# Kernel tuning notes

Hardware: AMD Instinct MI355X
Metric: run time of the kernel (lower is better)

The kernel has to match this reference:

```python
import jax, jax.numpy as jnp
import numpy as np

N, E, D, K, B = 50000, 600000, 128, 8, 64
E_DIM = 16  # edge_attr feature dim (hard-coded nn.Linear(16, in_dim))


def setup_inputs() -> dict:
    key = jax.random.key(0)
    ks = jax.random.split(key, 10)
    x = jax.random.normal(ks[0], (N, D), dtype=jnp.float32)
    edge_index = jax.random.randint(ks[1], (2, E), 0, N)
    edge_attr = jax.random.normal(ks[2], (E, E_DIM), dtype=jnp.float32)
    # binary pocket membership mask [N, K]
    pkt_mask = (jax.random.uniform(ks[3], (N, K)) < 0.3).astype(jnp.float32)
    batch = jnp.sort(jax.random.randint(ks[4], (N,), 0, B))
    s = 1.0 / np.sqrt(D)
    We = jax.random.normal(ks[5], (E_DIM, D), dtype=jnp.float32) * (1.0 / np.sqrt(E_DIM))
    be = jnp.zeros((D,), jnp.float32)
    W1 = jax.random.normal(ks[6], (D, D), dtype=jnp.float32) * s
    b1 = jnp.zeros((D,), jnp.float32)
    W2 = jax.random.normal(ks[7], (D, D), dtype=jnp.float32) * s
    b2 = jnp.zeros((D,), jnp.float32)
    eps = jnp.zeros((), jnp.float32)  # GINEConv train_eps init 0
    gamma = jnp.ones((D,), jnp.float32)
    beta = jnp.zeros((D,), jnp.float32)
    Wv = jax.random.normal(ks[8], (D, D), dtype=jnp.float32) * s
    bv = jnp.zeros((D,), jnp.float32)
    return {"x": x, "edge_index": edge_index, "edge_attr": edge_attr,
            "pkt_mask": pkt_mask, "batch": batch,
            "We": We, "be": be, "W1": W1, "b1": b1, "W2": W2, "b2": b2,
            "eps": eps, "gamma": gamma, "beta": beta, "Wv": Wv, "bv": bv}


def reference(x, edge_index, edge_attr, pkt_mask, batch,
              We, be, W1, b1, W2, b2, eps, gamma, beta, Wv, bv):
    src, dst = edge_index[0], edge_index[1]
    # edge_lin: [E,16] -> [E,D]
    edge_emb = edge_attr @ We + be
    # GINEConv: message = relu(x_src + edge_emb), scatter-add at dst
    msg = jax.nn.relu(x[src] + edge_emb)
    agg = jax.ops.segment_sum(msg, dst, num_segments=N)
    h = (1.0 + eps) * x + agg
    x_res = jax.nn.relu(h @ W1 + b1) @ W2 + b2  # nn MLP
    # virtual feedback: pocket-wise masked mean pooling per graph
    xw = x_res[:, None, :] * pkt_mask[:, :, None]          # [N,K,D]
    pocket_sum = jax.ops.segment_sum(xw.reshape(N, K * D), batch,
                                     num_segments=B).reshape(B, K, D)
    pocket_count = jax.ops.segment_sum(pkt_mask, batch, num_segments=B)  # [B,K]
    pocket_mean = pocket_sum / (pocket_count[:, :, None] + 1e-9)
    pocket_emb = pocket_mean @ Wv + bv                      # [B,K,D]
    node_pe = pocket_emb[batch]                             # gather -> [N,K,D]
    x_res = x_res + (node_pe * pkt_mask[:, :, None]).sum(axis=1)
    # LayerNorm (eps=1e-5, population variance as in torch)
    mu = x_res.mean(axis=-1, keepdims=True)
    var = ((x_res - mu) ** 2).mean(axis=-1, keepdims=True)
    y = (x_res - mu) / jnp.sqrt(var + 1e-5) * gamma + beta
    # ReLU activation; dropout is identity in eval mode
    return jax.nn.relu(y)
```

## Files before the change

kernel.cpp:

```cpp
#include <hip/hip_runtime.h>
#include <hip/hip_bf16.h>
#include <stdint.h>

#define D 128
#define K 8
#define BGRAPH 64
#define CH 64
#define GRP 4

__global__ __launch_bounds__(256) void cast_x_kernel(
    const float* __restrict__ x, __hip_bfloat16* __restrict__ xb, int n)
{
    const int i = (blockIdx.x * 256 + threadIdx.x) * 8;
    if (i + 8 > n) return;
    const float4 a = *(const float4*)(x + i);
    const float4 b = *(const float4*)(x + i + 4);
    __hip_bfloat16 v[8];
    v[0] = __float2bfloat16(a.x); v[1] = __float2bfloat16(a.y);
    v[2] = __float2bfloat16(a.z); v[3] = __float2bfloat16(a.w);
    v[4] = __float2bfloat16(b.x); v[5] = __float2bfloat16(b.y);
    v[6] = __float2bfloat16(b.z); v[7] = __float2bfloat16(b.w);
    *(uint4*)(xb + i) = *(const uint4*)v;
}

__global__ __launch_bounds__(256) void hist_kernel(
    const int* __restrict__ dst, int* __restrict__ deg, int E)
{
    const int i = (blockIdx.x * 256 + threadIdx.x) * 4;
    if (i + 4 <= E) {
        const int4 v = *(const int4*)(dst + i);
        atomicAdd(&deg[v.x], 1);
        atomicAdd(&deg[v.y], 1);
        atomicAdd(&deg[v.z], 1);
        atomicAdd(&deg[v.w], 1);
    } else {
        for (int j = i; j < E; ++j) atomicAdd(&deg[dst[j]], 1);
    }
}

__global__ __launch_bounds__(256) void scan_partial_kernel(
    const int* __restrict__ deg, int* __restrict__ bsum, int N)
{
    const int t = threadIdx.x;
    const int base = (blockIdx.x * 256 + t) * 4;
    int s = 0;
    if (base + 4 <= N) {
        const int4 v = *(const int4*)(deg + base);
        s = v.x + v.y + v.z + v.w;
    } else {
        for (int j = base; j < N; ++j) s += deg[j];
    }
    __shared__ int red[256];
    red[t] = s;
    __syncthreads();
    for (int off = 128; off; off >>= 1) {
        if (t < off) red[t] += red[t + off];
        __syncthreads();
    }
    if (t == 0) bsum[blockIdx.x] = red[0];
}

__global__ __launch_bounds__(64) void scan_top_kernel(
    const int* __restrict__ bsum, int* __restrict__ boffs, int nb)
{
    __shared__ int sh[64];
    const int t = threadIdx.x;
    const int v = (t < nb) ? bsum[t] : 0;
    sh[t] = v;
    __syncthreads();
    for (int off = 1; off < 64; off <<= 1) {
        const int u = (t >= off) ? sh[t - off] : 0;
        __syncthreads();
        sh[t] += u;
        __syncthreads();
    }
    if (t < nb) boffs[t] = sh[t] - v;
}

__global__ __launch_bounds__(256) void scan_final_kernel(
    const int* __restrict__ deg, const int* __restrict__ boffs,
    int* __restrict__ cursor, int N)
{
    const int t = threadIdx.x;
    const int base = (blockIdx.x * 256 + t) * 4;
    int v0 = 0, v1 = 0, v2 = 0, v3 = 0;
    if (base + 4 <= N) {
        const int4 v = *(const int4*)(deg + base);
        v0 = v.x; v1 = v.y; v2 = v.z; v3 = v.w;
    } else {
        if (base     < N) v0 = deg[base];
        if (base + 1 < N) v1 = deg[base + 1];
        if (base + 2 < N) v2 = deg[base + 2];
        if (base + 3 < N) v3 = deg[base + 3];
    }
    const int s = v0 + v1 + v2 + v3;
    __shared__ int sh[256];
    sh[t] = s;
    __syncthreads();
    for (int off = 1; off < 256; off <<= 1) {
        const int u = (t >= off) ? sh[t - off] : 0;
        __syncthreads();
        sh[t] += u;
        __syncthreads();
    }
    int ex = boffs[blockIdx.x] + sh[t] - s;
    if (base < N)     { cursor[base]     = ex; } ex += v0;
    if (base + 1 < N) { cursor[base + 1] = ex; } ex += v1;
    if (base + 2 < N) { cursor[base + 2] = ex; } ex += v2;
    if (base + 3 < N) { cursor[base + 3] = ex; }
}

__global__ __launch_bounds__(256) void scatter_kernel(
    const int* __restrict__ src, const int* __restrict__ dst,
    int* __restrict__ cursor, int4* __restrict__ sde, int E)
{
    const int i = blockIdx.x * 256 + threadIdx.x;
    if (i < E) {
        const int sv = src[i];
        const int dv = dst[i];
        const int p = atomicAdd(&cursor[dv], 1);
        sde[p] = make_int4(sv, dv, i, 0);
    }
}

__device__ __forceinline__ void flush_row(
    float* __restrict__ agg, int node, int d, float2 acc, int first, int last)
{
    float* p = agg + (size_t)node * D + d;
    if (node == first || node == last) {
        if (acc.x != 0.f) atomicAdd(p,     acc.x);
        if (acc.y != 0.f) atomicAdd(p + 1, acc.y);
    } else {
        *(float2*)p = acc;
    }
}

__global__ __launch_bounds__(256) void gine_reduce_kernel(
    const __hip_bfloat16* __restrict__ xb, const int4* __restrict__ sde,
    const float* __restrict__ ea, const float* __restrict__ We,
    const float* __restrict__ be, float* __restrict__ agg, int E)
{
    const int wave = threadIdx.x >> 6;
    const int lane = threadIdx.x & 63;
    const int chunk = __builtin_amdgcn_readfirstlane(blockIdx.x * 4 + wave);
    const int e0 = chunk * CH;
    if (e0 >= E) return;
    const int d = lane * 2;
    const int NG = CH / GRP;

    float2 w[16];
    #pragma unroll
    for (int j = 0; j < 16; ++j) w[j] = *(const float2*)(We + j * D + d);
    const float2 bb = *(const float2*)(be + d);

    int4 mcur[GRP], mnext[GRP];
    #pragma unroll
    for (int j = 0; j < GRP; ++j) mcur[j] = sde[e0 + j];
    #pragma unroll
    for (int j = 0; j < GRP; ++j) mnext[j] = sde[e0 + GRP + j];
    __hip_bfloat162 xcur[GRP];
    #pragma unroll
    for (int j = 0; j < GRP; ++j)
        xcur[j] = *(const __hip_bfloat162*)(xb + (size_t)mcur[j].x * D + d);

    const int first = mcur[0].y;
    const int last  = sde[e0 + CH - 1].y;

    float2 acc = make_float2(0.f, 0.f);
    int cur = first;

    for (int g = 0; g < NG; ++g) {
        int4 mnn[GRP] = {};
        __hip_bfloat162 xn[GRP] = {};
        if (g + 2 < NG) {
            #pragma unroll
            for (int j = 0; j < GRP; ++j) mnn[j] = sde[e0 + (g + 2) * GRP + j];
        }
        if (g + 1 < NG) {
            #pragma unroll
            for (int j = 0; j < GRP; ++j)
                xn[j] = *(const __hip_bfloat162*)(xb + (size_t)mnext[j].x * D + d);
        }

        float4 A[GRP][4];
        #pragma unroll
        for (int j = 0; j < GRP; ++j) {
            const float4* p = (const float4*)(ea + (size_t)mcur[j].z * 16);
            A[j][0] = p[0]; A[j][1] = p[1]; A[j][2] = p[2]; A[j][3] = p[3];
        }

        #pragma unroll
        for (int j = 0; j < GRP; ++j) {
            const int dk = mcur[j].y;
            if (dk != cur) {
                flush_row(agg, cur, d, acc, first, last);
                acc = make_float2(0.f, 0.f);
                cur = dk;
            }
            float m0 = bb.x + __bfloat162float(xcur[j].x);
            float m1 = bb.y + __bfloat162float(xcur[j].y);
            const float av[16] = {
                A[j][0].x, A[j][0].y, A[j][0].z, A[j][0].w,
                A[j][1].x, A[j][1].y, A[j][1].z, A[j][1].w,
                A[j][2].x, A[j][2].y, A[j][2].z, A[j][2].w,
                A[j][3].x, A[j][3].y, A[j][3].z, A[j][3].w};
            #pragma unroll
            for (int jj = 0; jj < 16; ++jj) {
                m0 += av[jj] * w[jj].x;
                m1 += av[jj] * w[jj].y;
            }
            acc.x += m0 > 0.f ? m0 : 0.f;
            acc.y += m1 > 0.f ? m1 : 0.f;
        }

        #pragma unroll
        for (int j = 0; j < GRP; ++j) {
            mcur[j] = mnext[j]; mnext[j] = mnn[j]; xcur[j] = xn[j];
        }
    }
    flush_row(agg, cur, d, acc, first, last);
}

#define MT_ROWS 64
#define SH_STR  132
__global__ __launch_bounds__(256) void mlp_kernel(
    const float* __restrict__ x, const float* __restrict__ agg,
    const float* __restrict__ epsp,
    const float* __restrict__ W1, const float* __restrict__ b1,
    const float* __restrict__ W2, const float* __restrict__ b2,
    float* __restrict__ xres, int N)
{
    __shared__ float sh[MT_ROWS * SH_STR];
    const int row0 = blockIdx.x * MT_ROWS;
    const float ep = 1.0f + epsp[0];

    for (int i = threadIdx.x; i < MT_ROWS * D / 4; i += 256) {
        const int flat = i * 4;
        const int r = flat >> 7;
        const int c = flat & (D - 1);
        const int row = row0 + r;
        float4 hv;
        if (row < N) {
            const float4 xv = *(const float4*)(x   + (size_t)row * D + c);
            const float4 av = *(const float4*)(agg + (size_t)row * D + c);
            hv = make_float4(ep * xv.x + av.x, ep * xv.y + av.y,
                             ep * xv.z + av.z, ep * xv.w + av.w);
        } else {
            hv = make_float4(0.f, 0.f, 0.f, 0.f);
        }
        *(float4*)(sh + r * SH_STR + c) = hv;
    }
    __syncthreads();

    const int cg = (threadIdx.x & 15) * 8;
    const int rg = (threadIdx.x >> 4) * 4;

    float acc[4][8];

    {
        const float4 bA = *(const float4*)(b1 + cg);
        const float4 bB = *(const float4*)(b1 + cg + 4);
        #pragma unroll
        for (int r = 0; r < 4; ++r) {
            acc[r][0] = bA.x; acc[r][1] = bA.y; acc[r][2] = bA.z; acc[r][3] = bA.w;
            acc[r][4] = bB.x; acc[r][5] = bB.y; acc[r][6] = bB.z; acc[r][7] = bB.w;
        }
        for (int k = 0; k < D; k += 4) {
            float wv[4][8];
            #pragma unroll
            for (int kk = 0; kk < 4; ++kk) {
                const float4 wa = *(const float4*)(W1 + (size_t)(k + kk) * D + cg);
                const float4 wb = *(const float4*)(W1 + (size_t)(k + kk) * D + cg + 4);
                wv[kk][0] = wa.x; wv[kk][1] = wa.y; wv[kk][2] = wa.z; wv[kk][3] = wa.w;
                wv[kk][4] = wb.x; wv[kk][5] = wb.y; wv[kk][6] = wb.z; wv[kk][7] = wb.w;
            }
            #pragma unroll
            for (int r = 0; r < 4; ++r) {
                const float4 h4 = *(const float4*)(sh + (rg + r) * SH_STR + k);
                const float hk[4] = {h4.x, h4.y, h4.z, h4.w};
                #pragma unroll
                for (int kk = 0; kk < 4; ++kk)
                    #pragma unroll
                    for (int c = 0; c < 8; ++c)
                        acc[r][c] += hk[kk] * wv[kk][c];
            }
        }
    }
    __syncthreads();

    #pragma unroll
    for (int r = 0; r < 4; ++r) {
        float4 oa, ob;
        oa.x = acc[r][0] > 0.f ? acc[r][0] : 0.f;
        oa.y = acc[r][1] > 0.f ? acc[r][1] : 0.f;
        oa.z = acc[r][2] > 0.f ? acc[r][2] : 0.f;
        oa.w = acc[r][3] > 0.f ? acc[r][3] : 0.f;
        ob.x = acc[r][4] > 0.f ? acc[r][4] : 0.f;
        ob.y = acc[r][5] > 0.f ? acc[r][5] : 0.f;
        ob.z = acc[r][6] > 0.f ? acc[r][6] : 0.f;
        ob.w = acc[r][7] > 0.f ? acc[r][7] : 0.f;
        *(float4*)(sh + (rg + r) * SH_STR + cg)     = oa;
        *(float4*)(sh + (rg + r) * SH_STR + cg + 4) = ob;
    }
    __syncthreads();

    {
        const float4 bA = *(const float4*)(b2 + cg);
        const float4 bB = *(const float4*)(b2 + cg + 4);
        #pragma unroll
        for (int r = 0; r < 4; ++r) {
            acc[r][0] = bA.x; acc[r][1] = bA.y; acc[r][2] = bA.z; acc[r][3] = bA.w;
            acc[r][4] = bB.x; acc[r][5] = bB.y; acc[r][6] = bB.z; acc[r][7] = bB.w;
        }
        for (int k = 0; k < D; k += 4) {
            float wv[4][8];
            #pragma unroll
            for (int kk = 0; kk < 4; ++kk) {
                const float4 wa = *(const float4*)(W2 + (size_t)(k + kk) * D + cg);
                const float4 wb = *(const float4*)(W2 + (size_t)(k + kk) * D + cg + 4);
                wv[kk][0] = wa.x; wv[kk][1] = wa.y; wv[kk][2] = wa.z; wv[kk][3] = wa.w;
                wv[kk][4] = wb.x; wv[kk][5] = wb.y; wv[kk][6] = wb.z; wv[kk][7] = wb.w;
            }
            #pragma unroll
            for (int r = 0; r < 4; ++r) {
                const float4 h4 = *(const float4*)(sh + (rg + r) * SH_STR + k);
                const float hk[4] = {h4.x, h4.y, h4.z, h4.w};
                #pragma unroll
                for (int kk = 0; kk < 4; ++kk)
                    #pragma unroll
                    for (int c = 0; c < 8; ++c)
                        acc[r][c] += hk[kk] * wv[kk][c];
            }
        }
        #pragma unroll
        for (int r = 0; r < 4; ++r) {
            const int row = row0 + rg + r;
            if (row < N) {
                *(float4*)(xres + (size_t)row * D + cg) =
                    make_float4(acc[r][0], acc[r][1], acc[r][2], acc[r][3]);
                *(float4*)(xres + (size_t)row * D + cg + 4) =
                    make_float4(acc[r][4], acc[r][5], acc[r][6], acc[r][7]);
            }
        }
    }
}

#define PPARTS 32
__global__ __launch_bounds__(128) void pocket_sum_kernel(
    const float* __restrict__ xres, const float* __restrict__ pmask,
    const int* __restrict__ batch,
    float* __restrict__ psum, float* __restrict__ pcnt, int N)
{
    const int g = blockIdx.x / PPARTS;
    const int part = blockIdx.x % PPARTS;

    int lo, hi;
    {
        int l = 0, r = N;
        while (l < r) { int m = (l + r) >> 1; if (batch[m] < g) l = m + 1; else r = m; }
        lo = l;
        r = N;
        while (l < r) { int m = (l + r) >> 1; if (batch[m] < g + 1) l = m + 1; else r = m; }
        hi = l;
    }
    const int cnt = hi - lo;
    const int per = (cnt + PPARTS - 1) / PPARTS;
    const int s = lo + part * per;
    const int e = min(s + per, hi);

    const int d = threadIdx.x;
    float acc[K];
    #pragma unroll
    for (int k = 0; k < K; ++k) acc[k] = 0.0f;
    float c = 0.0f;

    for (int n = s; n < e; ++n) {
        const float xv = xres[(size_t)n * D + d];
        const float4 m0 = *(const float4*)(pmask + (size_t)n * K);
        const float4 m1 = *(const float4*)(pmask + (size_t)n * K + 4);
        acc[0] += m0.x * xv; acc[1] += m0.y * xv;
        acc[2] += m0.z * xv; acc[3] += m0.w * xv;
        acc[4] += m1.x * xv; acc[5] += m1.y * xv;
        acc[6] += m1.z * xv; acc[7] += m1.w * xv;
        if (d < K) c += pmask[(size_t)n * K + d];
    }
    #pragma unroll
    for (int k = 0; k < K; ++k)
        atomicAdd(&psum[(size_t)g * (K * D) + k * D + d], acc[k]);
    if (d < K) atomicAdd(&pcnt[g * K + d], c);
}

__global__ __launch_bounds__(128) void pocket_emb_kernel(
    const float* __restrict__ psum, const float* __restrict__ pcnt,
    const float* __restrict__ Wv, const float* __restrict__ bv,
    float* __restrict__ pemb)
{
    __shared__ float smean[K * D];
    __shared__ float scnt[K];
    const int g = blockIdx.x;
    const int d = threadIdx.x;
    if (d < K) scnt[d] = pcnt[g * K + d];
    __syncthreads();
    #pragma unroll
    for (int k = 0; k < K; ++k)
        smean[k * D + d] = psum[(size_t)g * (K * D) + k * D + d] / (scnt[k] + 1e-9f);
    __syncthreads();

    float acc[K];
    const float bvv = bv[d];
    #pragma unroll
    for (int k = 0; k < K; ++k) acc[k] = bvv;
    for (int j = 0; j < D; ++j) {
        const float w = Wv[j * D + d];
        #pragma unroll
        for (int k = 0; k < K; ++k) acc[k] += smean[k * D + j] * w;
    }
    #pragma unroll
    for (int k = 0; k < K; ++k)
        pemb[(size_t)g * (K * D) + k * D + d] = acc[k];
}

__global__ __launch_bounds__(256) void ln_kernel(
    const float* __restrict__ xres, const float* __restrict__ pmask,
    const int* __restrict__ batch, const float* __restrict__ pemb,
    const float* __restrict__ gamma, const float* __restrict__ beta,
    float* __restrict__ out, int N)
{
    const int wave = threadIdx.x >> 6;
    const int lane = threadIdx.x & 63;
    const int n = blockIdx.x * 4 + wave;
    if (n >= N) return;
    const int d = lane * 2;

    float2 v = *(const float2*)(xres + (size_t)n * D + d);
    const int g = batch[n];
    const float* pe = pemb + (size_t)g * (K * D);
    const float4 m0 = *(const float4*)(pmask + (size_t)n * K);
    const float4 m1 = *(const float4*)(pmask + (size_t)n * K + 4);
    const float mk[K] = {m0.x, m0.y, m0.z, m0.w, m1.x, m1.y, m1.z, m1.w};
    #pragma unroll
    for (int k = 0; k < K; ++k) {
        if (mk[k] != 0.0f) {
            const float2 p = *(const float2*)(pe + k * D + d);
            v.x += mk[k] * p.x;
            v.y += mk[k] * p.y;
        }
    }

    float s = v.x + v.y;
    #pragma unroll
    for (int off = 32; off; off >>= 1) s += __shfl_xor(s, off, 64);
    const float mu = s * (1.0f / 128.0f);
    const float d0 = v.x - mu, d1 = v.y - mu;
    float sq = d0 * d0 + d1 * d1;
    #pragma unroll
    for (int off = 32; off; off >>= 1) sq += __shfl_xor(sq, off, 64);
    const float var = sq * (1.0f / 128.0f);
    const float inv = rsqrtf(var + 1e-5f);

    const float2 gm = *(const float2*)(gamma + d);
    const float2 bt = *(const float2*)(beta + d);
    float y0 = d0 * inv * gm.x + bt.x;
    float y1 = d1 * inv * gm.y + bt.y;
    y0 = y0 > 0.0f ? y0 : 0.0f;
    y1 = y1 > 0.0f ? y1 : 0.0f;
    *(float2*)(out + (size_t)n * D + d) = make_float2(y0, y1);
}

extern "C" void kernel_launch(void* const* d_in, const int* in_sizes, int n_in,
                              void* d_out, int out_size, void* d_ws, size_t ws_size,
                              hipStream_t stream)
{
    const float* x     = (const float*)d_in[0];
    const int*   ei    = (const int*)  d_in[1];
    const float* ea    = (const float*)d_in[2];
    const float* pmask = (const float*)d_in[3];
    const int*   batch = (const int*)  d_in[4];
    const float* We    = (const float*)d_in[5];
    const float* be    = (const float*)d_in[6];
    const float* W1    = (const float*)d_in[7];
    const float* b1    = (const float*)d_in[8];
    const float* W2    = (const float*)d_in[9];
    const float* b2    = (const float*)d_in[10];
    const float* epsp  = (const float*)d_in[11];
    const float* gamma = (const float*)d_in[12];
    const float* beta  = (const float*)d_in[13];
    const float* Wv    = (const float*)d_in[14];
    const float* bv    = (const float*)d_in[15];
    float* out = (float*)d_out;

    const int N = in_sizes[0] / D;
    const int E = in_sizes[1] / 2;
    const int* src = ei;
    const int* dst = ei + E;

    int*   deg  = (int*)d_ws;
    float* agg  = (float*)(deg + N);
    float* psum = agg + (size_t)N * D;
    float* pcnt = psum + (size_t)BGRAPH * K * D;
    float* xres = pcnt + (size_t)BGRAPH * K;
    float* pemb = xres + (size_t)N * D;
    float* extra = pemb + (size_t)BGRAPH * K * D;
    __hip_bfloat16* xb = (__hip_bfloat16*)(extra + 128);

    int*  cursor = (int*)xres;
    int4* sde    = (int4*)(((uintptr_t)(cursor + N) + 15) & ~(uintptr_t)15);
    int*  bsum   = (int*)extra;
    int*  boffs  = bsum + 64;

    const int nb = (N + 1023) / 1024;
    const int nchunks = (E + CH - 1) / CH;

    const size_t zero_bytes =
        ((size_t)N + (size_t)N * D + (size_t)BGRAPH * K * D + BGRAPH * K) * sizeof(float);
    hipMemsetAsync(d_ws, 0, zero_bytes, stream);

    cast_x_kernel<<<(N * D / 8 + 255) / 256, 256, 0, stream>>>(x, xb, N * D);
    hist_kernel<<<(E / 4 + 255) / 256, 256, 0, stream>>>(dst, deg, E);
    scan_partial_kernel<<<nb, 256, 0, stream>>>(deg, bsum, N);
    scan_top_kernel<<<1, 64, 0, stream>>>(bsum, boffs, nb);
    scan_final_kernel<<<nb, 256, 0, stream>>>(deg, boffs, cursor, N);
    scatter_kernel<<<(E + 255) / 256, 256, 0, stream>>>(src, dst, cursor, sde, E);
    gine_reduce_kernel<<<(nchunks + 3) / 4, 256, 0, stream>>>(
        xb, sde, ea, We, be, agg, E);

    mlp_kernel<<<(N + MT_ROWS - 1) / MT_ROWS, 256, 0, stream>>>(
        x, agg, epsp, W1, b1, W2, b2, xres, N);
    pocket_sum_kernel<<<BGRAPH * PPARTS, 128, 0, stream>>>(
        xres, pmask, batch, psum, pcnt, N);
    pocket_emb_kernel<<<BGRAPH, 128, 0, stream>>>(psum, pcnt, Wv, bv, pemb);
    ln_kernel<<<(N + 3) / 4, 256, 0, stream>>>(
        xres, pmask, batch, pemb, gamma, beta, out, N);
}
```

Before: 405.6 us.

## Run node MLP with bf16 MFMA and pre-transposed bf16 weights

Replaces the scalar fp32 two-layer MLP with a per-wave 16x16x32 bf16 MFMA implementation, converting the hidden activations to bf16 on the fly from shared memory. A new small kernel transposes and casts W1 and W2 to bf16 once per call. This targets the FMA-bound dense MLP cost at the price of reduced precision in both matmuls and less coalesced output stores.

New measurement: 376.4 us. 7.2% less time.

```diff
diff --git a/kernel.cpp b/kernel.cpp
--- a/kernel.cpp
+++ b/kernel.cpp
@@ -7,6 +7,15 @@
 #define BGRAPH 64
 #define CH 64
 #define GRP 4
+
+typedef __attribute__((ext_vector_type(8))) short bf16x8;
+typedef __attribute__((ext_vector_type(4))) float f32x4;
+
+__device__ __forceinline__ short f2bf(float f) {
+    union { float f; uint32_t u; } v; v.f = f;
+    const uint32_t r = (v.u + 0x7fffu + ((v.u >> 16) & 1u)) >> 16;
+    return (short)r;
+}
 
 __global__ __launch_bounds__(256) void cast_x_kernel(
     const float* __restrict__ x, __hip_bfloat16* __restrict__ xb, int n)
@@ -21,6 +30,18 @@
     v[4] = __float2bfloat16(b.x); v[5] = __float2bfloat16(b.y);
     v[6] = __float2bfloat16(b.z); v[7] = __float2bfloat16(b.w);
     *(uint4*)(xb + i) = *(const uint4*)v;
+}
+
+__global__ __launch_bounds__(128) void cast_w_kernel(
+    const float* __restrict__ W1, const float* __restrict__ W2,
+    short* __restrict__ wb1t, short* __restrict__ wb2t)
+{
+    const int which = blockIdx.x >> 7;
+    const int n = blockIdx.x & 127;
+    const int k = threadIdx.x;
+    const float* W = which ? W2 : W1;
+    short* O = which ? wb2t : wb1t;
+    O[n * D + k] = f2bf(W[(size_t)k * D + n]);
 }
 
 __global__ __launch_bounds__(256) void hist_kernel(
@@ -221,126 +242,97 @@
     flush_row(agg, cur, d, acc, first, last);
 }
 
-#define MT_ROWS 64
-#define SH_STR  132
-__global__ __launch_bounds__(256) void mlp_kernel(
+#define MROWS 64
+#define HSTR  132
+__global__ __launch_bounds__(256) void mlp_mfma_kernel(
     const float* __restrict__ x, const float* __restrict__ agg,
     const float* __restrict__ epsp,
-    const float* __restrict__ W1, const float* __restrict__ b1,
-    const float* __restrict__ W2, const float* __restrict__ b2,
+    const short* __restrict__ wb1t, const float* __restrict__ b1,
+    const short* __restrict__ wb2t, const float* __restrict__ b2,
     float* __restrict__ xres, int N)
 {
-    __shared__ float sh[MT_ROWS * SH_STR];
-    const int row0 = blockIdx.x * MT_ROWS;
+    __shared__ float hsh[MROWS * HSTR];
+    const int row0 = blockIdx.x * MROWS;
     const float ep = 1.0f + epsp[0];
 
-    for (int i = threadIdx.x; i < MT_ROWS * D / 4; i += 256) {
+    for (int i = threadIdx.x; i < MROWS * D / 4; i += 256) {
         const int flat = i * 4;
         const int r = flat >> 7;
         const int c = flat & (D - 1);
         const int row = row0 + r;
-        float4 hv;
+        float4 hv = make_float4(0.f, 0.f, 0.f, 0.f);
         if (row < N) {
             const float4 xv = *(const float4*)(x   + (size_t)row * D + c);
             const float4 av = *(const float4*)(agg + (size_t)row * D + c);
             hv = make_float4(ep * xv.x + av.x, ep * xv.y + av.y,
                              ep * xv.z + av.z, ep * xv.w + av.w);
-        } else {
-            hv = make_float4(0.f, 0.f, 0.f, 0.f);
-        }
-        *(float4*)(sh + r * SH_STR + c) = hv;
+        }
+        *(float4*)(hsh + r * HSTR + c) = hv;
     }
     __syncthreads();
 
-    const int cg = (threadIdx.x & 15) * 8;
-    const int rg = (threadIdx.x >> 4) * 4;
-
-    float acc[4][8];
-
-    {
-        const float4 bA = *(const float4*)(b1 + cg);
-        const float4 bB = *(const float4*)(b1 + cg + 4);
+    const int lane = threadIdx.x & 63;
+    const int wrow = (threadIdx.x >> 6) * 16;
+    const int m = lane & 15;
+    const int q = lane >> 4;
+
+    f32x4 acc[8];
+
+    #pragma unroll
+    for (int ct = 0; ct < 8; ++ct) {
+        const float b = b1[ct * 16 + m];
+        acc[ct] = (f32x4){b, b, b, b};
+    }
+    #pragma unroll
+    for (int ks = 0; ks < 4; ++ks) {
+        const float* ap = hsh + (wrow + m) * HSTR + ks * 32 + q * 8;
+        float av[8];
+        *(float4*)(av)     = *(const float4*)ap;
+        *(float4*)(av + 4) = *(const float4*)(ap + 4);
+        bf16x8 a;
+        #pragma unroll
+        for (int j = 0; j < 8; ++j) a[j] = f2bf(av[j]);
+        #pragma unroll
+        for (int ct = 0; ct < 8; ++ct) {
+            const bf16x8 b = *(const bf16x8*)(wb1t + (ct * 16 + m) * D + ks * 32 + q * 8);
+            acc[ct] = __builtin_amdgcn_mfma_f32_16x16x32_bf16(a, b, acc[ct], 0, 0, 0);
+        }
+    }
+    #pragma unroll
+    for (int ct = 0; ct < 8; ++ct)
         #pragma unroll
         for (int r = 0; r < 4; ++r) {
-            acc[r][0] = bA.x; acc[r][1] = bA.y; acc[r][2] = bA.z; acc[r][3] = bA.w;
-            acc[r][4] = bB.x; acc[r][5] = bB.y; acc[r][6] = bB.z; acc[r][7] = bB.w;
-        }
-        for (int k = 0; k < D; k += 4) {
-            float wv[4][8];
+            const float v = acc[ct][r];
+            hsh[(wrow + q * 4 + r) * HSTR + ct * 16 + m] = v > 0.f ? v : 0.f;
+        }
+
+    #pragma unroll
+    for (int ct = 0; ct < 8; ++ct) {
+        const float b = b2[ct * 16 + m];
+        acc[ct] = (f32x4){b, b, b, b};
+    }
+    #pragma unroll
+    for (int ks = 0; ks < 4; ++ks) {
+        const float* ap = hsh + (wrow + m) * HSTR + ks * 32 + q * 8;
+        float av[8];
+        *(float4*)(av)     = *(const float4*)ap;
+        *(float4*)(av + 4) = *(const float4*)(ap + 4);
+        bf16x8 a;
+        #pragma unroll
+        for (int j = 0; j < 8; ++j) a[j] = f2bf(av[j]);
+        #pragma unroll
+        for (int ct = 0; ct < 8; ++ct) {
+            const bf16x8 b = *(const bf16x8*)(wb2t + (ct * 16 + m) * D + ks * 32 + q * 8);
+            acc[ct] = __builtin_amdgcn_mfma_f32_16x16x32_bf16(a, b, acc[ct], 0, 0, 0);
+        }
+    }
+    #pragma unroll
+    for (int r = 0; r < 4; ++r) {
+        const int row = row0 + wrow + q * 4 + r;
+        if (row < N) {
             #pragma unroll
-            for (int kk = 0; kk < 4; ++kk) {
-                const float4 wa = *(const float4*)(W1 + (size_t)(k + kk) * D + cg);
-                const float4 wb = *(const float4*)(W1 + (size_t)(k + kk) * D + cg + 4);
-                wv[kk][0] = wa.x; wv[kk][1] = wa.y; wv[kk][2] = wa.z; wv[kk][3] = wa.w;
-                wv[kk][4] = wb.x; wv[kk][5] = wb.y; wv[kk][6] = wb.z; wv[kk][7] = wb.w;
-            }
-            #pragma unroll
-            for (int r = 0; r < 4; ++r) {
-                const float4 h4 = *(const float4*)(sh + (rg + r) * SH_STR + k);
-                const float hk[4] = {h4.x, h4.y, h4.z, h4.w};
-                #pragma unroll
-                for (int kk = 0; kk < 4; ++kk)
-                    #pragma unroll
-                    for (int c = 0; c < 8; ++c)
-                        acc[r][c] += hk[kk] * wv[kk][c];
-            }
-        }
-    }
-    __syncthreads();
-
-    #pragma unroll
-    for (int r = 0; r < 4; ++r) {
-        float4 oa, ob;
-        oa.x = acc[r][0] > 0.f ? acc[r][0] : 0.f;
-        oa.y = acc[r][1] > 0.f ? acc[r][1] : 0.f;
-        oa.z = acc[r][2] > 0.f ? acc[r][2] : 0.f;
-        oa.w = acc[r][3] > 0.f ? acc[r][3] : 0.f;
-        ob.x = acc[r][4] > 0.f ? acc[r][4] : 0.f;
-        ob.y = acc[r][5] > 0.f ? acc[r][5] : 0.f;
-        ob.z = acc[r][6] > 0.f ? acc[r][6] : 0.f;
-        ob.w = acc[r][7] > 0.f ? acc[r][7] : 0.f;
-        *(float4*)(sh + (rg + r) * SH_STR + cg)     = oa;
-        *(float4*)(sh + (rg + r) * SH_STR + cg + 4) = ob;
-    }
-    __syncthreads();
-
-    {
-        const float4 bA = *(const float4*)(b2 + cg);
-        const float4 bB = *(const float4*)(b2 + cg + 4);
-        #pragma unroll
-        for (int r = 0; r < 4; ++r) {
-            acc[r][0] = bA.x; acc[r][1] = bA.y; acc[r][2] = bA.z; acc[r][3] = bA.w;
-            acc[r][4] = bB.x; acc[r][5] = bB.y; acc[r][6] = bB.z; acc[r][7] = bB.w;
-        }
-        for (int k = 0; k < D; k += 4) {
-            float wv[4][8];
-            #pragma unroll
-            for (int kk = 0; kk < 4; ++kk) {
-                const float4 wa = *(const float4*)(W2 + (size_t)(k + kk) * D + cg);
-                const float4 wb = *(const float4*)(W2 + (size_t)(k + kk) * D + cg + 4);
-                wv[kk][0] = wa.x; wv[kk][1] = wa.y; wv[kk][2] = wa.z; wv[kk][3] = wa.w;
-                wv[kk][4] = wb.x; wv[kk][5] = wb.y; wv[kk][6] = wb.z; wv[kk][7] = wb.w;
-            }
-            #pragma unroll
-            for (int r = 0; r < 4; ++r) {
-                const float4 h4 = *(const float4*)(sh + (rg + r) * SH_STR + k);
-                const float hk[4] = {h4.x, h4.y, h4.z, h4.w};
-                #pragma unroll
-                for (int kk = 0; kk < 4; ++kk)
-                    #pragma unroll
-                    for (int c = 0; c < 8; ++c)
-                        acc[r][c] += hk[kk] * wv[kk][c];
-            }
-        }
-        #pragma unroll
-        for (int r = 0; r < 4; ++r) {
-            const int row = row0 + rg + r;
-            if (row < N) {
-                *(float4*)(xres + (size_t)row * D + cg) =
-                    make_float4(acc[r][0], acc[r][1], acc[r][2], acc[r][3]);
-                *(float4*)(xres + (size_t)row * D + cg + 4) =
-                    make_float4(acc[r][4], acc[r][5], acc[r][6], acc[r][7]);
-            }
+            for (int ct = 0; ct < 8; ++ct)
+                xres[(size_t)row * D + ct * 16 + m] = acc[ct][r];
         }
     }
 }
@@ -502,6 +494,8 @@
     float* pemb = xres + (size_t)N * D;
     float* extra = pemb + (size_t)BGRAPH * K * D;
     __hip_bfloat16* xb = (__hip_bfloat16*)(extra + 128);
+    short* wb1t = (short*)(xb + (size_t)N * D);
+    short* wb2t = wb1t + (size_t)D * D;
 
     int*  cursor = (int*)xres;
     int4* sde    = (int4*)(((uintptr_t)(cursor + N) + 15) & ~(uintptr_t)15);
@@ -516,6 +510,7 @@
     hipMemsetAsync(d_ws, 0, zero_bytes, stream);
 
     cast_x_kernel<<<(N * D / 8 + 255) / 256, 256, 0, stream>>>(x, xb, N * D);
+    cast_w_kernel<<<256, 128, 0, stream>>>(W1, W2, wb1t, wb2t);
     hist_kernel<<<(E / 4 + 255) / 256, 256, 0, stream>>>(dst, deg, E);
     scan_partial_kernel<<<nb, 256, 0, stream>>>(deg, bsum, N);
     scan_top_kernel<<<1, 64, 0, stream>>>(bsum, boffs, nb);
@@ -524,8 +519,8 @@
     gine_reduce_kernel<<<(nchunks + 3) / 4, 256, 0, stream>>>(
         xb, sde, ea, We, be, agg, E);
 
-    mlp_kernel<<<(N + MT_ROWS - 1) / MT_ROWS, 256, 0, stream>>>(
-        x, agg, epsp, W1, b1, W2, b2, xres, N);
+    mlp_mfma_kernel<<<(N + MROWS - 1) / MROWS, 256, 0, stream>>>(
+        x, agg, epsp, wb1t, b1, wb2t, b2, xres, N);
     pocket_sum_kernel<<<BGRAPH * PPARTS, 128, 0, stream>>>(
         xres, pmask, batch, psum, pcnt, N);
     pocket_emb_kernel<<<BGRAPH, 128, 0, stream>>>(psum, pcnt, Wv, bv, pemb);
```
